# Kernel optimization log

Measured on AMD Instinct MI355X. Metric: run time of the kernel, lower is better.

Reference implementation:

```python
import jax, jax.numpy as jnp
import numpy as np

B, T, E_A, E_B, E_ATT, N_HEAD = 2, 2048, 2048, 2048, 2048, 16
HS = E_ATT // N_HEAD  # 128
ROPE_BASE = 100000.0


def setup_inputs() -> dict:
    key = jax.random.key(0)
    ks = jax.random.split(key, 6)
    Ta = T // 2
    x_a = jax.random.normal(ks[0], (B, Ta, E_A), jnp.float32)
    x_b = jax.random.normal(ks[1], (B, T - Ta, E_B), jnp.float32)
    # alternating text/other tokens: even positions are stream-a
    mask_a = jnp.tile((jnp.arange(T) % 2 == 0)[None, :], (B, 1))
    # standard RoPE tables, full head_size (freqs duplicated), as litgpt/nanoGPT build them
    pos = jnp.arange(T, dtype=jnp.float32)
    inv_freq = 1.0 / (ROPE_BASE ** (jnp.arange(0, HS, 2, dtype=jnp.float32) / HS))
    freqs = pos[:, None] * inv_freq[None, :]           # [T, HS/2]
    emb = jnp.concatenate([freqs, freqs], axis=-1)      # [T, HS]
    cos, sin = jnp.cos(emb), jnp.sin(emb)
    s = 0.02
    Wqkv_a = jax.random.normal(ks[2], (E_A, 3 * E_ATT), jnp.float32) * s
    Wqkv_b = jax.random.normal(ks[3], (E_B, 3 * E_ATT), jnp.float32) * s
    Wproj_a = jax.random.normal(ks[4], (E_ATT, E_A), jnp.float32) * s
    Wproj_b = jax.random.normal(ks[5], (E_ATT, E_B), jnp.float32) * s
    return dict(x_a=x_a, x_b=x_b, cos=cos, sin=sin, mask_a=mask_a,
                Wqkv_a=Wqkv_a, Wqkv_b=Wqkv_b, Wproj_a=Wproj_a, Wproj_b=Wproj_b)


def _apply_rope(x, cos, sin):
    # x: [B, H, T, HS]; cos/sin: [T, HS] broadcast over leading dims
    x1 = x[..., : HS // 2]
    x2 = x[..., HS // 2:]
    rot = jnp.concatenate([-x2, x1], axis=-1)
    return (x * cos + rot * sin).astype(x.dtype)


def reference(x_a, x_b, cos, sin, mask_a, Wqkv_a, Wqkv_b, Wproj_a, Wproj_b):
    Bm, Tm = mask_a.shape
    Na = x_a.shape[0] * x_a.shape[1]  # static token counts per stream
    Nb = x_b.shape[0] * x_b.shape[1]
    C3 = Wqkv_a.shape[1]              # 3 * E_ATT
    # dual-stream QKV projections (bias=False)
    qkv_a = (x_a @ Wqkv_a).reshape(-1, C3)
    qkv_b = (x_b @ Wqkv_b).reshape(-1, C3)
    # interleave tokens back into the full [B, T] layout by mask scatter
    flat = mask_a.reshape(-1)
    idx_a = jnp.nonzero(flat, size=Na)[0]
    idx_b = jnp.nonzero(~flat, size=Nb)[0]
    kqv = jnp.zeros((Bm * Tm, C3), qkv_a.dtype).at[idx_a].set(qkv_a).at[idx_b].set(qkv_b)
    kqv = kqv.reshape(Bm, Tm, 3 * N_HEAD, HS).transpose(0, 2, 1, 3)  # [B, 3H, T, hs]
    q, k, v = kqv[:, :N_HEAD], kqv[:, N_HEAD:2 * N_HEAD], kqv[:, 2 * N_HEAD:]
    q = _apply_rope(q, cos, sin)
    k = _apply_rope(k, cos, sin)
    # causal SDPA (dropout_p = 0 at eval)
    scale = 1.0 / np.sqrt(HS).astype(np.float32)
    att = jnp.einsum('bhqd,bhkd->bhqk', q, k) * scale
    causal = jnp.tril(jnp.ones((Tm, Tm), bool))
    att = jnp.where(causal, att, -jnp.inf)
    att = jax.nn.softmax(att, axis=-1)
    y = jnp.einsum('bhqk,bhkd->bhqd', att, v)
    y = y.transpose(0, 2, 1, 3).reshape(Bm * Tm, N_HEAD * HS)
    # mask split + per-stream output projections
    y_a = y[idx_a] @ Wproj_a
    y_b = y[idx_b] @ Wproj_b
    return (y_a, y_b)
```

## Files before the change

### kernel.cpp

```cpp
#include <hip/hip_runtime.h>
#include <hip/hip_bf16.h>


typedef __attribute__((ext_vector_type(8))) short v8s;
typedef __attribute__((ext_vector_type(4))) float v4f;

#define GL2LDS(gptr, lptr)                                              \
  __builtin_amdgcn_global_load_lds(                                     \
      (const __attribute__((address_space(1))) void*)(gptr),            \
      (__attribute__((address_space(3))) void*)(lptr), 16, 0, 0)

#define S_BARRIER() asm volatile("s_barrier" ::: "memory")

__device__ __forceinline__ float b2f(unsigned short u) {
  return __uint_as_float(((unsigned int)u) << 16);
}
__device__ __forceinline__ unsigned short f2bf(float f) {
  unsigned int u = __float_as_uint(f);
  u += 0x7fffu + ((u >> 16) & 1u);
  return (unsigned short)(u >> 16);
}

__global__ __launch_bounds__(256) void f32_to_bf16_2(
    const float4* __restrict__ a, const float4* __restrict__ b,
    uint2* __restrict__ out, int n4each) {
  int i = blockIdx.x * 256 + threadIdx.x;
  if (i >= 2 * n4each) return;
  float4 v = (i < n4each) ? a[i] : b[i - n4each];
  uint2 o;
  o.x = (unsigned int)f2bf(v.x) | ((unsigned int)f2bf(v.y) << 16);
  o.y = (unsigned int)f2bf(v.z) | ((unsigned int)f2bf(v.w) << 16);
  out[i] = o;
}

__global__ __launch_bounds__(256) void transpose_f32_bf16(
    const float* __restrict__ in0, const float* __restrict__ in1,
    unsigned short* __restrict__ out0, unsigned short* __restrict__ out1,
    int R, int C) {
  const float* in = blockIdx.z ? in1 : in0;
  unsigned short* out = blockIdx.z ? out1 : out0;
  __shared__ unsigned short tile[64][65];
  const int bc = blockIdx.x * 64, br = blockIdx.y * 64;
  const int c  = threadIdx.x & 63;
  const int r0 = threadIdx.x >> 6;
  for (int r = r0; r < 64; r += 4)
    tile[r][c] = f2bf(in[(size_t)(br + r) * C + bc + c]);
  __syncthreads();
  for (int rr = r0; rr < 64; rr += 4)
    out[(size_t)(bc + rr) * R + br + c] = tile[c][rr];
}

template <int MH, int NH>
__device__ __forceinline__ void mfma_quad(v4f (&acc)[8][4], const v8s (&a)[4][2],
                                          const v8s (&b)[4][2]) {
  __builtin_amdgcn_s_setprio(1);
#pragma unroll
  for (int ks = 0; ks < 2; ++ks)
#pragma unroll
    for (int i = 0; i < 4; ++i)
#pragma unroll
      for (int j = 0; j < 2; ++j)
        acc[MH * 4 + i][NH * 2 + j] = __builtin_amdgcn_mfma_f32_16x16x32_bf16(
            a[i][ks], b[NH * 2 + j][ks], acc[MH * 4 + i][NH * 2 + j], 0, 0, 0);
  __builtin_amdgcn_s_setprio(0);
}

__device__ __forceinline__ void read_a_half(const unsigned short* lds, int base,
                                            int mh, int r, int c0, int c1,
                                            v8s (&a)[4][2]) {
#pragma unroll
  for (int i = 0; i < 4; ++i) {
    const unsigned short* ap = lds + base + (mh * 64 + i * 16 + r) * 64;
    a[i][0] = *(const v8s*)(ap + c0);
    a[i][1] = *(const v8s*)(ap + c1);
  }
}

template <int NH>
__device__ __forceinline__ void read_b_half(const unsigned short* lds, int base,
                                            int brow, int r, int c0, int c1,
                                            v8s (&b)[4][2]) {
#pragma unroll
  for (int j = 0; j < 2; ++j) {
    const unsigned short* bp = lds + base + (brow + (NH * 2 + j) * 16 + r) * 64;
    b[NH * 2 + j][0] = *(const v8s*)(bp + c0);
    b[NH * 2 + j][1] = *(const v8s*)(bp + c1);
  }
}

template <int GATHER, int OSCAT>
__global__ __launch_bounds__(512, 2) void gemm256(
    const unsigned short* __restrict__ A,
    const unsigned short* __restrict__ BT0,
    const unsigned short* __restrict__ BT1,
    void* __restrict__ Cout, int M, int N, int K, int NBN) {
  __shared__ __align__(16) unsigned short lds[65536];
  const int tid = threadIdx.x;
  const int par = blockIdx.y;
  const unsigned short* __restrict__ BT = par ? BT1 : BT0;

  int wg = blockIdx.x;
  const int cpx = gridDim.x >> 3;
  wg = (wg & 7) * cpx + (wg >> 3);
  const int m0 = (wg / NBN) * 256, n0 = (wg % NBN) * 256;

  const int w = tid >> 6, lane = tid & 63;
  const int wm = w >> 2, wn = w & 3;
  const int r = lane & 15, q = lane >> 4;
  const int rs = r & 7;
  const int c0 = ((q ^ rs) << 3);
  const int c1 = (((4 + q) ^ rs) << 3);
  const int brow = (wn & 1) << 6;
  const int AbaseE = (2 + wm) * 8192, BbaseE = (wn >> 1) * 8192;
  const int AbaseO = (6 + wm) * 8192, BbaseO = (4 + (wn >> 1)) * 8192;

  const int sr0 = tid >> 3, sslot = tid & 7;
  const int NT = K >> 6, NIT = NT >> 1;

  auto stageB = [&](int p, int tt) {
    unsigned short* dst = &lds[(((tt << 2) + p) & 7) * 8192 + w * 512];
#pragma unroll
    for (int cc = 0; cc < 2; ++cc) {
      const int row = sr0 + cc * 64;
      const int g = ((sslot ^ (row & 7)) << 3);
      GL2LDS(BT + (size_t)(n0 + p * 128 + row) * K + tt * 64 + g, dst + cc * 4096);
    }
  };
  auto stageA = [&](int p, int tt) {
    unsigned short* dst = &lds[(((tt << 2) + 2 + p) & 7) * 8192 + w * 512];
#pragma unroll
    for (int cc = 0; cc < 2; ++cc) {
      const int row = sr0 + cc * 64;
      const int g = ((sslot ^ (row & 7)) << 3);
      int ar = m0 + p * 128 + row;
      if constexpr (GATHER) ar = ((ar >> 10) << 11) + ((ar & 1023) << 1) + par;
      GL2LDS(A + (size_t)ar * K + tt * 64 + g, dst + cc * 4096);
    }
  };

  v4f acc[8][4] = {};
  v8s a[4][2], b[4][2];

  stageB(0, 0); stageB(1, 0); stageA(0, 0); stageA(1, 0);
  asm volatile("" ::: "memory");
  stageB(0, 1); stageB(1, 1);
  asm volatile("s_waitcnt vmcnt(4)" ::: "memory");
  S_BARRIER();

  for (int it = 0; it < NIT; ++it) {
    const int t = it << 1;
    const bool more = (it + 1 < NIT);

    read_a_half(lds, AbaseE, 0, r, c0, c1, a);
    read_b_half<0>(lds, BbaseE, brow, r, c0, c1, b);
    stageA(0, t + 1);
    S_BARRIER();
    mfma_quad<0, 0>(acc, a, b);
    S_BARRIER();
    read_b_half<1>(lds, BbaseE, brow, r, c0, c1, b);
    stageA(1, t + 1);
    S_BARRIER();
    mfma_quad<0, 1>(acc, a, b);
    S_BARRIER();
    read_a_half(lds, AbaseE, 1, r, c0, c1, a);
    if (more) stageB(0, t + 2);
    S_BARRIER();
    mfma_quad<1, 0>(acc, a, b);
    S_BARRIER();
    if (more) stageB(1, t + 2);
    S_BARRIER();
    mfma_quad<1, 1>(acc, a, b);
    if (more) { asm volatile("s_waitcnt vmcnt(4)" ::: "memory"); }
    else      { asm volatile("s_waitcnt vmcnt(0)" ::: "memory"); }
    S_BARRIER();

    read_a_half(lds, AbaseO, 0, r, c0, c1, a);
    read_b_half<0>(lds, BbaseO, brow, r, c0, c1, b);
    if (more) stageA(0, t + 2);
    S_BARRIER();
    mfma_quad<0, 0>(acc, a, b);
    S_BARRIER();
    read_b_half<1>(lds, BbaseO, brow, r, c0, c1, b);
    if (more) stageA(1, t + 2);
    S_BARRIER();
    mfma_quad<0, 1>(acc, a, b);
    S_BARRIER();
    read_a_half(lds, AbaseO, 1, r, c0, c1, a);
    if (more) stageB(0, t + 3);
    S_BARRIER();
    mfma_quad<1, 0>(acc, a, b);
    S_BARRIER();
    if (more) stageB(1, t + 3);
    S_BARRIER();
    mfma_quad<1, 1>(acc, a, b);
    if (more) { asm volatile("s_waitcnt vmcnt(4)" ::: "memory"); }
    S_BARRIER();
  }

  float* Cf = (float*)Cout + (size_t)par * M * N;
  unsigned short* Cb = (unsigned short*)Cout;
#pragma unroll
  for (int tm = 0; tm < 8; ++tm) {
    const int rowm = m0 + wm * 128 + tm * 16 + q * 4;
#pragma unroll
    for (int tn = 0; tn < 4; ++tn) {
      const int col = n0 + wn * 64 + tn * 16 + r;
#pragma unroll
      for (int p = 0; p < 4; ++p) {
        if constexpr (OSCAT == 0) {
          Cf[(size_t)(rowm + p) * N + col] = acc[tm][tn][p];
        } else {
          const int ar = rowm + p;
          const int orow = ((ar >> 10) << 11) + ((ar & 1023) << 1) + (OSCAT - 1);
          Cb[(size_t)orow * N + col] = f2bf(acc[tm][tn][p]);
        }
      }
    }
  }
}

__global__ __launch_bounds__(256) void scatter_rope(
    const unsigned short* __restrict__ qkv,
    const float* __restrict__ cosb, const float* __restrict__ sinb,
    unsigned short* __restrict__ Q, unsigned short* __restrict__ K) {
  const int token = blockIdx.x;
  const int b = token >> 11, t = token & 2047;
  const unsigned short* src = qkv + (size_t)token * 6144;
  for (int i = threadIdx.x; i < 2048; i += 256) {
    const int d = i & 127, h = i >> 7;
    const float cv = cosb[t * 128 + d];
    const float sv = sinb[t * 128 + d];
    const int   mate = (d < 64) ? i + 64 : i - 64;
    const float sgn  = (d < 64) ? -1.f : 1.f;
    const float qv = b2f(src[i]),        qm = b2f(src[mate]) * sgn;
    const float kv = b2f(src[2048 + i]), km = b2f(src[2048 + mate]) * sgn;
    const size_t off = ((size_t)(b * 16 + h) * 2048 + t) * 128 + d;
    Q[off] = f2bf(qv * cv + qm * sv);
    K[off] = f2bf(kv * cv + km * sv);
  }
}

__global__ __launch_bounds__(256) void transpose_v(
    const unsigned short* __restrict__ qkv, unsigned short* __restrict__ Vt) {
  __shared__ unsigned short tile[128][129];
  const int bh = blockIdx.x >> 4, tt = blockIdx.x & 15;
  const int b = bh >> 4, h = bh & 15;
  const int tid = threadIdx.x;
  const int d0 = tid & 127, t0 = tid >> 7;
#pragma unroll 4
  for (int i = 0; i < 64; ++i) {
    int tl = i * 2 + t0;
    tile[tl][d0] =
        qkv[((size_t)(b * 2048 + tt * 128 + tl)) * 6144 + 4096 + h * 128 + d0];
  }
  __syncthreads();
#pragma unroll 4
  for (int i = 0; i < 64; ++i) {
    int dd = i * 2 + t0;
    Vt[((size_t)(bh * 128 + dd)) * 2048 + tt * 128 + d0] = tile[d0][dd];
  }
}

#define SIG 0.1275174038536989f

__global__ __launch_bounds__(256, 2) void attn_flash(
    const unsigned short* __restrict__ Q, const unsigned short* __restrict__ K,
    const unsigned short* __restrict__ Vt, unsigned short* __restrict__ Y) {
  __shared__ __align__(16) unsigned short Ks[2][64 * 128];
  __shared__ __align__(16) unsigned short Vs[2][128 * 64];
  __shared__ __align__(16) unsigned short Pl[64 * 72];

  const int x = blockIdx.x;
  const int bh = (x & 7) * 4 + ((x >> 3) & 3);
  const int pr = x >> 5;
  const int tid = threadIdx.x, w = tid >> 6, lane = tid & 63;
  const int r = lane & 15, q = lane >> 4;
  const int b = bh >> 4, h = bh & 15;
  const size_t kbase = (size_t)bh * 2048 * 128;
  const size_t vbase = (size_t)bh * 128 * 2048;
  const int vrow = lane >> 3, pc = lane & 7;

  for (int ph = 0; ph < 2; ++ph) {
    const int qt = ph ? pr : (31 - pr);

    const size_t qbase = ((size_t)bh * 2048 + qt * 64) * 128;
    v8s qf[4];
#pragma unroll
    for (int ki = 0; ki < 4; ++ki)
      qf[ki] = *(const v8s*)&Q[qbase + (size_t)(w * 16 + r) * 128 +
                               (ki * 4 + q) * 8];

    float mrun[4], lrun[4];
    v4f O[8] = {};
#pragma unroll
    for (int p = 0; p < 4; ++p) { mrun[p] = -3.0e38f; lrun[p] = 0.f; }

    const int nkt = qt + 1;

    auto stageKV = [&](int kt, int buf) {
#pragma unroll
      for (int i = 0; i < 4; ++i) {
        const int key = w * 16 + i * 4 + q;
        const int gs = r ^ (key & 15);
        GL2LDS(K + kbase + ((size_t)kt * 64 + key) * 128 + gs * 8,
               &Ks[buf][(w * 16 + i * 4) * 128]);
      }
#pragma unroll
      for (int i = 0; i < 4; ++i) {
        const int d = w * 32 + i * 8 + vrow;
        const int gs = pc ^ (d & 7);
        GL2LDS(Vt + vbase + (size_t)d * 2048 + kt * 64 + gs * 8,
               &Vs[buf][(w * 32 + i * 8) * 64]);
      }
    };

    stageKV(0, 0);
    for (int kt = 0; kt < nkt; ++kt) {
      const int buf = kt & 1;
      if (kt + 1 < nkt) {
        stageKV(kt + 1, buf ^ 1);
        asm volatile("s_waitcnt vmcnt(8)" ::: "memory");
      } else {
        asm volatile("s_waitcnt vmcnt(0)" ::: "memory");
      }
      S_BARRIER();

      v4f S[4] = {};
      __builtin_amdgcn_s_setprio(1);
#pragma unroll
      for (int ki = 0; ki < 4; ++ki) {
        v8s kf[4];
#pragma unroll
        for (int tn = 0; tn < 4; ++tn) {
          const int key = tn * 16 + r;
          const int c = (ki * 4 + q) ^ r;
          kf[tn] = *(const v8s*)&Ks[buf][key * 128 + c * 8];
        }
#pragma unroll
        for (int tn = 0; tn < 4; ++tn)
          S[tn] = __builtin_amdgcn_mfma_f32_16x16x32_bf16(
              qf[ki], kf[tn], S[tn], 0, 0, 0);
      }
      __builtin_amdgcn_s_setprio(0);

      if (kt == qt) {
#pragma unroll
        for (int tn = 0; tn < 4; ++tn)
#pragma unroll
          for (int p = 0; p < 4; ++p) {
            const int tq = w * 16 + q * 4 + p;
            const int kg = tn * 16 + r;
            if (kg > tq) S[tn][p] = -3.0e38f;
          }
      }

      float mxp[4];
      int need = 0;
#pragma unroll
      for (int p = 0; p < 4; ++p) {
        mxp[p] = fmaxf(fmaxf(S[0][p], S[1][p]), fmaxf(S[2][p], S[3][p]));
        need |= (mxp[p] > mrun[p] + 60.0f) ? 1 : 0;
      }

      if (__builtin_expect(__any(need), 0)) {
#pragma unroll
        for (int p = 0; p < 4; ++p) {
          float mx = mxp[p];
#pragma unroll
          for (int o = 1; o < 16; o <<= 1) mx = fmaxf(mx, __shfl_xor(mx, o, 64));
          const float mnew = fmaxf(mrun[p], mx);
          const float alpha = exp2f((mrun[p] - mnew) * SIG);
          mrun[p] = mnew;
          float psum = 0.f;
#pragma unroll
          for (int tn = 0; tn < 4; ++tn) {
            const float pv = exp2f((S[tn][p] - mnew) * SIG);
            S[tn][p] = pv;
            psum += pv;
          }
          lrun[p] = lrun[p] * alpha + psum;
#pragma unroll
          for (int tn = 0; tn < 8; ++tn) O[tn][p] *= alpha;
        }
      } else {
#pragma unroll
        for (int p = 0; p < 4; ++p) {
          float psum = 0.f;
#pragma unroll
          for (int tn = 0; tn < 4; ++tn) {
            const float pv = exp2f((S[tn][p] - mrun[p]) * SIG);
            S[tn][p] = pv;
            psum += pv;
          }
          lrun[p] += psum;
        }
      }

#pragma unroll
      for (int tn = 0; tn < 4; ++tn)
#pragma unroll
        for (int p = 0; p < 4; ++p) {
          const int m = w * 16 + q * 4 + p;
          Pl[m * 72 + tn * 16 + r] = f2bf(S[tn][p]);
        }

      __builtin_amdgcn_s_setprio(1);
#pragma unroll
      for (int ki = 0; ki < 2; ++ki) {
        v8s pf, vf[8];
        const int m = w * 16 + r;
        pf = *(const v8s*)&Pl[m * 72 + (ki * 4 + q) * 8];
#pragma unroll
        for (int tn = 0; tn < 8; ++tn) {
          const int d = tn * 16 + r;
          const int c = (ki * 4 + q) ^ (d & 7);
          vf[tn] = *(const v8s*)&Vs[buf][d * 64 + c * 8];
        }
#pragma unroll
        for (int tn = 0; tn < 8; ++tn)
          O[tn] = __builtin_amdgcn_mfma_f32_16x16x32_bf16(
              pf, vf[tn], O[tn], 0, 0, 0);
      }
      __builtin_amdgcn_s_setprio(0);

      asm volatile("s_waitcnt lgkmcnt(0)" ::: "memory");
      S_BARRIER();
    }

#pragma unroll
    for (int p = 0; p < 4; ++p) {
      float s = lrun[p];
#pragma unroll
      for (int o = 1; o < 16; o <<= 1) s += __shfl_xor(s, o, 64);
      const float inv = 1.0f / s;
      const int t = qt * 64 + w * 16 + q * 4 + p;
#pragma unroll
      for (int tn = 0; tn < 8; ++tn)
        Y[((size_t)(b * 2048 + t)) * 2048 + h * 128 + tn * 16 + r] =
            f2bf(O[tn][p] * inv);
    }
  }
}

extern "C" void kernel_launch(void* const* d_in, const int* in_sizes, int n_in,
                              void* d_out, int out_size, void* d_ws, size_t ws_size,
                              hipStream_t stream) {
  const float* x_a   = (const float*)d_in[0];
  const float* x_b   = (const float*)d_in[1];
  const float* cosb  = (const float*)d_in[2];
  const float* sinb  = (const float*)d_in[3];
  const float* Wqkv_a  = (const float*)d_in[5];
  const float* Wqkv_b  = (const float*)d_in[6];
  const float* Wproj_a = (const float*)d_in[7];
  const float* Wproj_b = (const float*)d_in[8];
  float* out = (float*)d_out;

  if (ws_size < 100663296u) return;

  char* ws = (char*)d_ws;
  unsigned short* QKVall = (unsigned short*)(ws);
  unsigned short* XA     = (unsigned short*)(ws + 50331648);
  unsigned short* WQT    = (unsigned short*)(ws + 67108864);
  unsigned short* Qb     = (unsigned short*)(ws + 50331648);
  unsigned short* Kb     = (unsigned short*)(ws + 67108864);
  unsigned short* Vtb    = (unsigned short*)(ws + 83886080);
  unsigned short* Yb     = (unsigned short*)(ws);
  unsigned short* WPT_A  = (unsigned short*)(ws + 16777216);
  unsigned short* WPT_B  = (unsigned short*)(ws + 25165824);

  hipLaunchKernelGGL(f32_to_bf16_2, dim3(8192), dim3(256), 0, stream,
                     (const float4*)x_a, (const float4*)x_b, (uint2*)XA, 1048576);
  hipLaunchKernelGGL(transpose_f32_bf16, dim3(96, 32, 1), dim3(256), 0, stream,
                     Wqkv_a, Wqkv_a, WQT, WQT, 2048, 6144);
  hipLaunchKernelGGL((gemm256<0, 1>), dim3(192, 1), dim3(512), 0, stream,
                     XA, WQT, WQT, QKVall, 2048, 6144, 2048, 24);
  hipLaunchKernelGGL(transpose_f32_bf16, dim3(96, 32, 1), dim3(256), 0, stream,
                     Wqkv_b, Wqkv_b, WQT, WQT, 2048, 6144);
  hipLaunchKernelGGL((gemm256<0, 2>), dim3(192, 1), dim3(512), 0, stream,
                     XA + (size_t)4194304, WQT, WQT, QKVall, 2048, 6144, 2048, 24);

  hipLaunchKernelGGL(scatter_rope, dim3(4096), dim3(256), 0, stream,
                     QKVall, cosb, sinb, Qb, Kb);
  hipLaunchKernelGGL(transpose_v, dim3(512), dim3(256), 0, stream,
                     QKVall, Vtb);

  hipLaunchKernelGGL(transpose_f32_bf16, dim3(32, 32, 2), dim3(256), 0, stream,
                     Wproj_a, Wproj_b, WPT_A, WPT_B, 2048, 2048);

  hipLaunchKernelGGL(attn_flash, dim3(512), dim3(256), 0, stream,
                     Qb, Kb, Vtb, Yb);

  hipLaunchKernelGGL((gemm256<1, 0>), dim3(64, 2), dim3(512), 0, stream,
                     Yb, WPT_A, WPT_B, out, 2048, 2048, 2048, 8);
}
```

Measured before the change: 472.0 us.

## Merge prep kernels, vectorize rope/V transpose, retile projection GEMM to 256x128

The x-cast and the Wqkv_a transpose become one launch, and RoPE plus the V transpose become another. RoPE and the V transpose now use 16-byte vector loads and stores. The Wproj transposes ride along as extra blocks in the attention launch so they can overlap the attention tail. The output projection moves to a new 256x128-tile GEMM with 256 blocks instead of 128, which fills more CUs. Together these aim to cut launch overhead and idle compute units, at the cost of more complex mixed-role kernels.

```diff
diff --git a/kernel.cpp b/kernel.cpp
--- a/kernel.cpp
+++ b/kernel.cpp
@@ -21,24 +21,36 @@
   return (unsigned short)(u >> 16);
 }
 
-__global__ __launch_bounds__(256) void f32_to_bf16_2(
-    const float4* __restrict__ a, const float4* __restrict__ b,
-    uint2* __restrict__ out, int n4each) {
-  int i = blockIdx.x * 256 + threadIdx.x;
-  if (i >= 2 * n4each) return;
-  float4 v = (i < n4each) ? a[i] : b[i - n4each];
-  uint2 o;
-  o.x = (unsigned int)f2bf(v.x) | ((unsigned int)f2bf(v.y) << 16);
-  o.y = (unsigned int)f2bf(v.z) | ((unsigned int)f2bf(v.w) << 16);
-  out[i] = o;
+__global__ __launch_bounds__(256) void prep_a(
+    const float4* __restrict__ xa, const float4* __restrict__ xb,
+    uint2* __restrict__ XA, const float* __restrict__ Wq,
+    unsigned short* __restrict__ WQT) {
+  __shared__ unsigned short tile[64][65];
+  const int bid = blockIdx.x, tid = threadIdx.x;
+  if (bid < 8192) {
+    const int n4each = 1048576;
+    int i = bid * 256 + tid;
+    if (i >= 2 * n4each) return;
+    float4 v = (i < n4each) ? xa[i] : xb[i - n4each];
+    uint2 o;
+    o.x = (unsigned int)f2bf(v.x) | ((unsigned int)f2bf(v.y) << 16);
+    o.y = (unsigned int)f2bf(v.z) | ((unsigned int)f2bf(v.w) << 16);
+    XA[i] = o;
+    return;
+  }
+  const int id = bid - 8192;
+  const int bc = (id % 96) * 64, br = (id / 96) * 64;
+  const int c = tid & 63, r0 = tid >> 6;
+  for (int r = r0; r < 64; r += 4)
+    tile[r][c] = f2bf(Wq[(size_t)(br + r) * 6144 + bc + c]);
+  __syncthreads();
+  for (int rr = r0; rr < 64; rr += 4)
+    WQT[(size_t)(bc + rr) * 2048 + br + c] = tile[c][rr];
 }
 
 __global__ __launch_bounds__(256) void transpose_f32_bf16(
-    const float* __restrict__ in0, const float* __restrict__ in1,
-    unsigned short* __restrict__ out0, unsigned short* __restrict__ out1,
+    const float* __restrict__ in, unsigned short* __restrict__ out,
     int R, int C) {
-  const float* in = blockIdx.z ? in1 : in0;
-  unsigned short* out = blockIdx.z ? out1 : out0;
   __shared__ unsigned short tile[64][65];
   const int bc = blockIdx.x * 64, br = blockIdx.y * 64;
   const int c  = threadIdx.x & 63;
@@ -88,16 +100,13 @@
   }
 }
 
-template <int GATHER, int OSCAT>
+template <int OSCAT>
 __global__ __launch_bounds__(512, 2) void gemm256(
     const unsigned short* __restrict__ A,
-    const unsigned short* __restrict__ BT0,
-    const unsigned short* __restrict__ BT1,
-    void* __restrict__ Cout, int M, int N, int K, int NBN) {
+    const unsigned short* __restrict__ BT,
+    unsigned short* __restrict__ Cb, int M, int N, int K, int NBN) {
   __shared__ __align__(16) unsigned short lds[65536];
   const int tid = threadIdx.x;
-  const int par = blockIdx.y;
-  const unsigned short* __restrict__ BT = par ? BT1 : BT0;
 
   int wg = blockIdx.x;
   const int cpx = gridDim.x >> 3;
@@ -132,9 +141,7 @@
     for (int cc = 0; cc < 2; ++cc) {
       const int row = sr0 + cc * 64;
       const int g = ((sslot ^ (row & 7)) << 3);
-      int ar = m0 + p * 128 + row;
-      if constexpr (GATHER) ar = ((ar >> 10) << 11) + ((ar & 1023) << 1) + par;
-      GL2LDS(A + (size_t)ar * K + tt * 64 + g, dst + cc * 4096);
+      GL2LDS(A + (size_t)(m0 + p * 128 + row) * K + tt * 64 + g, dst + cc * 4096);
     }
   };
 
@@ -197,8 +204,6 @@
     S_BARRIER();
   }
 
-  float* Cf = (float*)Cout + (size_t)par * M * N;
-  unsigned short* Cb = (unsigned short*)Cout;
 #pragma unroll
   for (int tm = 0; tm < 8; ++tm) {
     const int rowm = m0 + wm * 128 + tm * 16 + q * 4;
@@ -207,73 +212,233 @@
       const int col = n0 + wn * 64 + tn * 16 + r;
 #pragma unroll
       for (int p = 0; p < 4; ++p) {
-        if constexpr (OSCAT == 0) {
-          Cf[(size_t)(rowm + p) * N + col] = acc[tm][tn][p];
-        } else {
-          const int ar = rowm + p;
-          const int orow = ((ar >> 10) << 11) + ((ar & 1023) << 1) + (OSCAT - 1);
-          Cb[(size_t)orow * N + col] = f2bf(acc[tm][tn][p]);
+        const int ar = rowm + p;
+        const int orow = ((ar >> 10) << 11) + ((ar & 1023) << 1) + (OSCAT - 1);
+        Cb[(size_t)orow * N + col] = f2bf(acc[tm][tn][p]);
+      }
+    }
+  }
+}
+
+__global__ __launch_bounds__(512, 2) void gemm_proj2(
+    const unsigned short* __restrict__ A,
+    const unsigned short* __restrict__ BT0,
+    const unsigned short* __restrict__ BT1,
+    float* __restrict__ out, int K) {
+  __shared__ __align__(16) unsigned short lds[65536];
+  const int tid = threadIdx.x;
+
+  int wg = blockIdx.x;
+  const int cpx = gridDim.x >> 3;
+  wg = (wg & 7) * cpx + (wg >> 3);
+  const int m0 = (wg >> 4) * 256, n0 = (wg & 15) * 128;
+  const int par = m0 >> 11;
+  const unsigned short* __restrict__ BT = par ? BT1 : BT0;
+
+  const int w = tid >> 6, lane = tid & 63;
+  const int wm = w >> 1, wn = w & 1;
+  const int r = lane & 15, q = lane >> 4;
+  const int rs = r & 7;
+  const int c0 = ((q ^ rs) << 3);
+  const int c1 = (((4 + q) ^ rs) << 3);
+
+  const int sr0 = tid >> 3, sslot = tid & 7;
+  const int NT = K >> 6, NIT = NT >> 1;
+
+  auto stageAh = [&](int ih, int tt) {
+    unsigned short* dst = &lds[(((tt & 1) << 2) + ih) * 8192 + w * 512];
+#pragma unroll
+    for (int cc = 0; cc < 2; ++cc) {
+      const int row = sr0 + cc * 64;
+      const int g = ((sslot ^ (row & 7)) << 3);
+      const int lr = (m0 + ih * 128 + row) & 2047;
+      const int gr = ((lr >> 10) << 11) + ((lr & 1023) << 1) + par;
+      GL2LDS(A + (size_t)gr * K + tt * 64 + g, dst + cc * 4096);
+    }
+  };
+  auto stageBh = [&](int tt) {
+    unsigned short* dst = &lds[(((tt & 1) << 2) + 2) * 8192 + w * 512];
+#pragma unroll
+    for (int cc = 0; cc < 2; ++cc) {
+      const int row = sr0 + cc * 64;
+      const int g = ((sslot ^ (row & 7)) << 3);
+      GL2LDS(BT + (size_t)(n0 + row) * K + tt * 64 + g, dst + cc * 4096);
+    }
+  };
+
+  v4f acc[4][4] = {};
+  v8s a[4][2], b[4][2];
+
+  auto readA = [&](int ih2, int t) {
+    const int base = (((t & 1) << 2) + (wm >> 1)) * 8192;
+#pragma unroll
+    for (int ii = 0; ii < 2; ++ii) {
+      const int i = ih2 * 2 + ii;
+      const unsigned short* ap = lds + base + ((wm & 1) * 64 + i * 16 + r) * 64;
+      a[i][0] = *(const v8s*)(ap + c0);
+      a[i][1] = *(const v8s*)(ap + c1);
+    }
+  };
+  auto readB = [&](int jh2, int t) {
+    const int base = (((t & 1) << 2) + 2) * 8192;
+#pragma unroll
+    for (int jj = 0; jj < 2; ++jj) {
+      const int j = jh2 * 2 + jj;
+      const unsigned short* bp = lds + base + (wn * 64 + j * 16 + r) * 64;
+      b[j][0] = *(const v8s*)(bp + c0);
+      b[j][1] = *(const v8s*)(bp + c1);
+    }
+  };
+  auto quad = [&](int ih, int jh) {
+    __builtin_amdgcn_s_setprio(1);
+#pragma unroll
+    for (int ks = 0; ks < 2; ++ks)
+#pragma unroll
+      for (int ii = 0; ii < 2; ++ii)
+#pragma unroll
+        for (int jj = 0; jj < 2; ++jj) {
+          const int i = ih * 2 + ii, j = jh * 2 + jj;
+          acc[i][j] = __builtin_amdgcn_mfma_f32_16x16x32_bf16(
+              a[i][ks], b[j][ks], acc[i][j], 0, 0, 0);
         }
-      }
-    }
-  }
-}
-
-__global__ __launch_bounds__(256) void scatter_rope(
+    __builtin_amdgcn_s_setprio(0);
+  };
+
+  stageAh(0, 0); stageAh(1, 0); stageBh(0);
+  asm volatile("" ::: "memory");
+  stageBh(1);
+  asm volatile("s_waitcnt vmcnt(2)" ::: "memory");
+  S_BARRIER();
+
+  for (int u = 0; u < NIT; ++u) {
+    const int t = 2 * u;
+    const bool more = (u + 1 < NIT);
+
+    readA(0, t); readB(0, t); stageAh(0, t + 1);
+    S_BARRIER(); quad(0, 0); S_BARRIER();
+    readB(1, t); stageAh(1, t + 1);
+    S_BARRIER(); quad(0, 1); S_BARRIER();
+    readA(1, t); if (more) stageBh(t + 2);
+    S_BARRIER(); quad(1, 0); quad(1, 1);
+    if (more) { asm volatile("s_waitcnt vmcnt(2)" ::: "memory"); }
+    else      { asm volatile("s_waitcnt vmcnt(0)" ::: "memory"); }
+    S_BARRIER();
+
+    readA(0, t + 1); readB(0, t + 1); if (more) stageAh(0, t + 2);
+    S_BARRIER(); quad(0, 0); S_BARRIER();
+    readB(1, t + 1); if (more) stageAh(1, t + 2);
+    S_BARRIER(); quad(0, 1); S_BARRIER();
+    readA(1, t + 1); if (more) stageBh(t + 3);
+    S_BARRIER(); quad(1, 0); quad(1, 1);
+    if (more) { asm volatile("s_waitcnt vmcnt(2)" ::: "memory"); }
+    S_BARRIER();
+  }
+
+  float* Cf = out + (size_t)par * 4194304;
+#pragma unroll
+  for (int i = 0; i < 4; ++i) {
+    const int lrow0 = (m0 & 2047) + wm * 64 + i * 16 + q * 4;
+#pragma unroll
+    for (int j = 0; j < 4; ++j) {
+      const int col = n0 + wn * 64 + j * 16 + r;
+#pragma unroll
+      for (int p = 0; p < 4; ++p)
+        Cf[(size_t)(lrow0 + p) * 2048 + col] = acc[i][j][p];
+    }
+  }
+}
+
+__global__ __launch_bounds__(256) void rope_tv(
     const unsigned short* __restrict__ qkv,
     const float* __restrict__ cosb, const float* __restrict__ sinb,
-    unsigned short* __restrict__ Q, unsigned short* __restrict__ K) {
-  const int token = blockIdx.x;
-  const int b = token >> 11, t = token & 2047;
-  const unsigned short* src = qkv + (size_t)token * 6144;
-  for (int i = threadIdx.x; i < 2048; i += 256) {
-    const int d = i & 127, h = i >> 7;
-    const float cv = cosb[t * 128 + d];
-    const float sv = sinb[t * 128 + d];
-    const int   mate = (d < 64) ? i + 64 : i - 64;
-    const float sgn  = (d < 64) ? -1.f : 1.f;
-    const float qv = b2f(src[i]),        qm = b2f(src[mate]) * sgn;
-    const float kv = b2f(src[2048 + i]), km = b2f(src[2048 + mate]) * sgn;
-    const size_t off = ((size_t)(b * 16 + h) * 2048 + t) * 128 + d;
-    Q[off] = f2bf(qv * cv + qm * sv);
-    K[off] = f2bf(kv * cv + km * sv);
-  }
-}
-
-__global__ __launch_bounds__(256) void transpose_v(
-    const unsigned short* __restrict__ qkv, unsigned short* __restrict__ Vt) {
-  __shared__ unsigned short tile[128][129];
-  const int bh = blockIdx.x >> 4, tt = blockIdx.x & 15;
+    unsigned short* __restrict__ Q, unsigned short* __restrict__ K,
+    unsigned short* __restrict__ Vt) {
+  __shared__ unsigned short tile[128][136];
+  const int tid = threadIdx.x;
+  if (blockIdx.x < 4096) {
+    const int token = blockIdx.x;
+    const int b = token >> 11, t = token & 2047;
+    const unsigned short* src = qkv + (size_t)token * 6144;
+    const int e0 = tid * 8, d0 = e0 & 127, h = e0 >> 7;
+    const int mate0 = (d0 < 64) ? e0 + 64 : e0 - 64;
+    const float sgn = (d0 < 64) ? -1.f : 1.f;
+    const v8s qo = *(const v8s*)&src[e0];
+    const v8s qm = *(const v8s*)&src[mate0];
+    const v8s ko = *(const v8s*)&src[2048 + e0];
+    const v8s km = *(const v8s*)&src[2048 + mate0];
+    const float4 ca = *(const float4*)&cosb[t * 128 + d0];
+    const float4 cb2 = *(const float4*)&cosb[t * 128 + d0 + 4];
+    const float4 sa = *(const float4*)&sinb[t * 128 + d0];
+    const float4 sb2 = *(const float4*)&sinb[t * 128 + d0 + 4];
+    const float cv[8] = {ca.x, ca.y, ca.z, ca.w, cb2.x, cb2.y, cb2.z, cb2.w};
+    const float sv[8] = {sa.x, sa.y, sa.z, sa.w, sb2.x, sb2.y, sb2.z, sb2.w};
+    v8s qout, kout;
+#pragma unroll
+    for (int j = 0; j < 8; ++j) {
+      qout[j] = (short)f2bf(b2f((unsigned short)qo[j]) * cv[j] +
+                            b2f((unsigned short)qm[j]) * sgn * sv[j]);
+      kout[j] = (short)f2bf(b2f((unsigned short)ko[j]) * cv[j] +
+                            b2f((unsigned short)km[j]) * sgn * sv[j]);
+    }
+    const size_t off = ((size_t)(b * 16 + h) * 2048 + t) * 128 + d0;
+    *(v8s*)&Q[off] = qout;
+    *(v8s*)&K[off] = kout;
+    return;
+  }
+  const int id = blockIdx.x - 4096;
+  const int bh = id >> 4, tt = id & 15;
   const int b = bh >> 4, h = bh & 15;
-  const int tid = threadIdx.x;
-  const int d0 = tid & 127, t0 = tid >> 7;
-#pragma unroll 4
-  for (int i = 0; i < 64; ++i) {
-    int tl = i * 2 + t0;
-    tile[tl][d0] =
-        qkv[((size_t)(b * 2048 + tt * 128 + tl)) * 6144 + 4096 + h * 128 + d0];
+  const int s = tid & 15, g0 = tid >> 4;
+#pragma unroll
+  for (int ps = 0; ps < 8; ++ps) {
+    const int tl = ps * 16 + g0;
+    *(v8s*)&tile[tl][s * 8] =
+        *(const v8s*)&qkv[((size_t)(b * 2048 + tt * 128 + tl)) * 6144 + 4096 +
+                          h * 128 + s * 8];
   }
   __syncthreads();
-#pragma unroll 4
-  for (int i = 0; i < 64; ++i) {
-    int dd = i * 2 + t0;
-    Vt[((size_t)(bh * 128 + dd)) * 2048 + tt * 128 + d0] = tile[d0][dd];
+#pragma unroll
+  for (int ps = 0; ps < 8; ++ps) {
+    const int dd = ps * 16 + g0;
+    v8s o;
+#pragma unroll
+    for (int j = 0; j < 8; ++j) o[j] = (short)tile[s * 8 + j][dd];
+    *(v8s*)&Vt[((size_t)(bh * 128 + dd)) * 2048 + tt * 128 + s * 8] = o;
   }
 }
 
 #define SIG 0.1275174038536989f
 
-__global__ __launch_bounds__(256, 2) void attn_flash(
+__global__ __launch_bounds__(256, 2) void attn_wpt(
     const unsigned short* __restrict__ Q, const unsigned short* __restrict__ K,
-    const unsigned short* __restrict__ Vt, unsigned short* __restrict__ Y) {
+    const unsigned short* __restrict__ Vt, unsigned short* __restrict__ Y,
+    const float* __restrict__ Wpa, const float* __restrict__ Wpb,
+    unsigned short* __restrict__ WTa, unsigned short* __restrict__ WTb) {
   __shared__ __align__(16) unsigned short Ks[2][64 * 128];
   __shared__ __align__(16) unsigned short Vs[2][128 * 64];
   __shared__ __align__(16) unsigned short Pl[64 * 72];
 
+  const int tid = threadIdx.x;
+  if (blockIdx.x >= 512) {
+    const int id = blockIdx.x - 512;
+    const int z = id >> 10, id2 = id & 1023;
+    const float* in = z ? Wpb : Wpa;
+    unsigned short* outp = z ? WTb : WTa;
+    unsigned short* tile = &Ks[0][0];
+    const int bc = (id2 & 31) * 64, br = (id2 >> 5) * 64;
+    const int c = tid & 63, r0 = tid >> 6;
+    for (int r = r0; r < 64; r += 4)
+      tile[r * 65 + c] = f2bf(in[(size_t)(br + r) * 2048 + bc + c]);
+    __syncthreads();
+    for (int rr = r0; rr < 64; rr += 4)
+      outp[(size_t)(bc + rr) * 2048 + br + c] = tile[c * 65 + rr];
+    return;
+  }
+
   const int x = blockIdx.x;
   const int bh = (x & 7) * 4 + ((x >> 3) & 3);
   const int pr = x >> 5;
-  const int tid = threadIdx.x, w = tid >> 6, lane = tid & 63;
+  const int w = tid >> 6, lane = tid & 63;
   const int r = lane & 15, q = lane >> 4;
   const int b = bh >> 4, h = bh & 15;
   const size_t kbase = (size_t)bh * 2048 * 128;
@@ -468,28 +633,19 @@
   unsigned short* WPT_A  = (unsigned short*)(ws + 16777216);
   unsigned short* WPT_B  = (unsigned short*)(ws + 25165824);
 
-  hipLaunchKernelGGL(f32_to_bf16_2, dim3(8192), dim3(256), 0, stream,
-                     (const float4*)x_a, (const float4*)x_b, (uint2*)XA, 1048576);
-  hipLaunchKernelGGL(transpose_f32_bf16, dim3(96, 32, 1), dim3(256), 0, stream,
-                     Wqkv_a, Wqkv_a, WQT, WQT, 2048, 6144);
-  hipLaunchKernelGGL((gemm256<0, 1>), dim3(192, 1), dim3(512), 0, stream,
-                     XA, WQT, WQT, QKVall, 2048, 6144, 2048, 24);
-  hipLaunchKernelGGL(transpose_f32_bf16, dim3(96, 32, 1), dim3(256), 0, stream,
-                     Wqkv_b, Wqkv_b, WQT, WQT, 2048, 6144);
-  hipLaunchKernelGGL((gemm256<0, 2>), dim3(192, 1), dim3(512), 0, stream,
-                     XA + (size_t)4194304, WQT, WQT, QKVall, 2048, 6144, 2048, 24);
-
-  hipLaunchKernelGGL(scatter_rope, dim3(4096), dim3(256), 0, stream,
-                     QKVall, cosb, sinb, Qb, Kb);
-  hipLaunchKernelGGL(transpose_v, dim3(512), dim3(256), 0, stream,
-                     QKVall, Vtb);
-
-  hipLaunchKernelGGL(transpose_f32_bf16, dim3(32, 32, 2), dim3(256), 0, stream,
-                     Wproj_a, Wproj_b, WPT_A, WPT_B, 2048, 2048);
-
-  hipLaunchKernelGGL(attn_flash, dim3(512), dim3(256), 0, stream,
-                     Qb, Kb, Vtb, Yb);
-
-  hipLaunchKernelGGL((gemm256<1, 0>), dim3(64, 2), dim3(512), 0, stream,
-                     Yb, WPT_A, WPT_B, out, 2048, 2048, 2048, 8);
-}
+  hipLaunchKernelGGL(prep_a, dim3(11264), dim3(256), 0, stream,
+                     (const float4*)x_a, (const float4*)x_b, (uint2*)XA,
+                     Wqkv_a, WQT);
+  hipLaunchKernelGGL((gemm256<1>), dim3(192), dim3(512), 0, stream,
+                     XA, WQT, QKVall, 2048, 6144, 2048, 24);
+  hipLaunchKernelGGL(transpose_f32_bf16, dim3(96, 32), dim3(256), 0, stream,
+                     Wqkv_b, WQT, 2048, 6144);
+  hipLaunchKernelGGL((gemm256<2>), dim3(192), dim3(512), 0, stream,
+                     XA + (size_t)4194304, WQT, QKVall, 2048, 6144, 2048, 24);
+  hipLaunchKernelGGL(rope_tv, dim3(4608), dim3(256), 0, stream,
+                     QKVall, cosb, sinb, Qb, Kb, Vtb);
+  hipLaunchKernelGGL(attn_wpt, dim3(2560), dim3(256), 0, stream,
+                     Qb, Kb, Vtb, Yb, Wproj_a, Wproj_b, WPT_A, WPT_B);
+  hipLaunchKernelGGL(gemm_proj2, dim3(256), dim3(512), 0, stream,
+                     Yb, WPT_A, WPT_B, out, 2048);
+}
```

After: 445.2 us. 1.06x faster.
